# Kernel tuning notes

Hardware: AMD Instinct MI355X
Metric: run time of the kernel (lower is better)

## Reference

```python
import jax, jax.numpy as jnp
import numpy as np
from jax.ops import segment_sum

N_NODE, N_EDGE, D_IN, D_HID, N_CLS = 50000, 800000, 64, 64, 40


def setup_inputs() -> dict:
    key = jax.random.key(0)
    k1, k2, k3, k4 = jax.random.split(key, 4)
    x = jax.random.normal(k1, (N_NODE, D_IN), dtype=jnp.float32)
    edge_index = jax.random.randint(k2, (2, N_EDGE), 0, N_NODE, dtype=jnp.int64)
    W1 = jax.random.normal(k3, (D_IN, D_HID), dtype=jnp.float32) * (1.0 / np.sqrt(D_IN))
    b1 = jnp.zeros((D_HID,), dtype=jnp.float32)
    W2 = jax.random.normal(k4, (D_HID, N_CLS), dtype=jnp.float32) * (1.0 / np.sqrt(D_HID))
    b2 = jnp.zeros((N_CLS,), dtype=jnp.float32)
    return {"x": x, "edge_index": edge_index, "W1": W1, "b1": b1, "W2": W2, "b2": b2}


def _att_weights(fea, row, col, n):
    # edge-parallel cosine similarity (sklearn cosine_similarity restricted to edges)
    nrm = jnp.sqrt(jnp.sum(fea * fea, axis=1, keepdims=True))
    fn = fea / jnp.maximum(nrm, 1e-12)
    sim = jnp.sum(fn[row] * fn[col], axis=1)                 # [E]
    sim = jnp.where(sim < 0.1, 0.0, sim)                      # threshold
    # L1 row-normalization (sim >= 0 after threshold)
    rs = segment_sum(sim, row, num_segments=n)                # [N]
    sim_n = jnp.where(sim > 0, sim / jnp.maximum(rs[row], 1e-12), 0.0)
    # degree-based self-loop weight lam = 1/(deg+1)
    deg = segment_sum((sim > 0).astype(fea.dtype), row, num_segments=n)
    lam = 1.0 / (deg + 1.0)
    # exp applied only to stored (nonzero) entries; zeroed edges stay 0
    w_edge = jnp.where(sim > 0, jnp.exp(sim_n), 0.0)          # [E]
    w_self = jnp.exp(lam)                                     # [N] self-loop weights
    return w_edge, w_self


def _gcn(h, W, b, row, col, w_edge, w_self, n):
    # symmetric-norm GCN over weighted edges + explicit self loops
    deg = segment_sum(w_edge, row, num_segments=n) + w_self
    dinv = 1.0 / jnp.sqrt(jnp.maximum(deg, 1e-12))
    h = h @ W                                                 # [N, F]
    coef = w_edge * dinv[row] * dinv[col]                     # [E]
    out = segment_sum(coef[:, None] * h[col], row, num_segments=n)
    out = out + (w_self * dinv * dinv)[:, None] * h + b
    return out


def reference(x, edge_index, W1, b1, W2, b2):
    n = x.shape[0]
    row, col = edge_index[0], edge_index[1]
    # layer 1: attention coefs from raw features
    w1e, w1s = _att_weights(x, row, col, n)
    h = jax.nn.relu(_gcn(x, W1, b1, row, col, w1e, w1s, n))
    # layer 2: attention coefs recomputed on hidden features (dropout = eval mode)
    w2e, w2s = _att_weights(h, row, col, n)
    out = _gcn(h, W2, b2, row, col, w2e, w2s, n)
    return jax.nn.log_softmax(out, axis=1)
```

## Files before the change

kernel.cpp:

```cpp
#include <hip/hip_runtime.h>
#include <math.h>


#define ATT_CAP 96
#define EPB     2048
#define RPB     32
#define NBUCK_MAX 1600
#define CAPB    1024

typedef _Float16 half4 __attribute__((ext_vector_type(4)));

__global__ void k_bscat_norm_gemm(const int* __restrict__ row, const int* __restrict__ col,
                                  int* __restrict__ gcur, int* __restrict__ ebuf,
                                  int E, int nbuck, int nblkA, int nblkB,
                                  const float* __restrict__ x, float* __restrict__ fn,
                                  const float* __restrict__ W1, float* __restrict__ hd1,
                                  int N)
{
    __shared__ float smem[64 * 64 + 4 * 64];
    int b = blockIdx.x;
    int tid = threadIdx.x;
    if (b >= nblkA + nblkB) {
        float* sW = smem;
        float* sX = smem + 64 * 64;
        int gb = b - nblkA - nblkB;
        const float4* W4 = (const float4*)W1;
        float4* s4 = (float4*)sW;
#pragma unroll
        for (int i = 0; i < 4; ++i) s4[tid + 256 * i] = W4[tid + 256 * i];
        int base = gb * 4;
        {
            int rr = base + (tid >> 6);
            sX[tid] = (rr < N) ? x[(unsigned)rr * 64u + (unsigned)(tid & 63)] : 0.0f;
        }
        __syncthreads();
        int rl = tid >> 6, j = tid & 63;
        int r = base + rl;
        if (r < N) {
            float acc = 0.0f;
#pragma unroll
            for (int k = 0; k < 64; ++k) acc = fmaf(sX[rl * 64 + k], sW[k * 64 + j], acc);
            hd1[(unsigned)r * 64u + (unsigned)j] = acc;
        }
        return;
    }
    if (b >= nblkA) {
        int gid  = (b - nblkA) * blockDim.x + tid;
        int wid  = gid >> 6;
        int lane = tid & 63;
        if (wid >= N) return;
        float v = x[(unsigned)wid * 64u + (unsigned)lane];
        float s = v * v;
#pragma unroll
        for (int off = 32; off > 0; off >>= 1) s += __shfl_xor(s, off);
        float inv = rsqrtf(fmaxf(s, 1e-24f));
        fn[(unsigned)wid * 64u + (unsigned)lane] = v * inv;
        return;
    }
    int* lh    = (int*)smem;
    int* lbase = lh + NBUCK_MAX;
    int ebeg = b * EPB;
    int rr[8], cc[8];
    for (int i = tid; i < nbuck; i += blockDim.x) lh[i] = 0;
    __syncthreads();
#pragma unroll
    for (int k = 0; k < 8; ++k) {
        int e = ebeg + k * 256 + tid;
        bool v = (e < E);
        int r = v ? row[e] : -1;
        int c = v ? col[e] : 0;
        rr[k] = r; cc[k] = c;
        if (v) atomicAdd(&lh[r >> 5], 1);
    }
    __syncthreads();
    for (int i = tid; i < nbuck; i += blockDim.x) {
        int cnt = lh[i];
        if (cnt) lbase[i] = i * CAPB + atomicAdd(gcur + i, cnt);
        lh[i] = 0;
    }
    __syncthreads();
#pragma unroll
    for (int k = 0; k < 8; ++k) {
        int r = rr[k];
        if (r >= 0) {
            int j = r >> 5;
            int pos = lbase[j] + atomicAdd(&lh[j], 1);
            ebuf[pos] = ((r & (RPB - 1)) << 16) | cc[k];
        }
    }
}

__global__ void k_csr(const int* __restrict__ ebuf, const int* __restrict__ gcur,
                      int* __restrict__ rptr, int* __restrict__ col_s,
                      int N, int E, int nbuck)
{
    __shared__ int pk[CAPB];
    __shared__ int lcol[CAPB];
    __shared__ int lcnt[RPB], lexc[RPB], lcur[RPB];
    __shared__ int spart[4];
    int j = blockIdx.x;
    int tid = threadIdx.x;
    int lane = tid & 63, wave = tid >> 6;

    int part = 0;
    for (int i = tid; i < j; i += blockDim.x) part += gcur[i];
#pragma unroll
    for (int off = 32; off > 0; off >>= 1) part += __shfl_xor(part, off);
    if (lane == 0) spart[wave] = part;
    if (tid < RPB) lcnt[tid] = 0;
    __syncthreads();
    int beg = spart[0] + spart[1] + spart[2] + spart[3];
    int m = gcur[j]; if (m > CAPB) m = CAPB;

    const int* seg = ebuf + (size_t)j * CAPB;
    for (int i = tid; i < m; i += blockDim.x) pk[i] = seg[i];
    __syncthreads();
    for (int i = tid; i < m; i += blockDim.x) atomicAdd(&lcnt[pk[i] >> 16], 1);
    __syncthreads();
    if (tid < 32) {
        int a = lcnt[tid];
        int incl = a;
#pragma unroll
        for (int off = 1; off < 32; off <<= 1) {
            int v = __shfl_up(incl, off);
            if (tid >= off) incl += v;
        }
        lexc[tid] = incl - a;
        lcur[tid] = incl - a;
    }
    __syncthreads();
    for (int i = tid; i < m; i += blockDim.x) {
        int v = pk[i];
        int p = atomicAdd(&lcur[v >> 16], 1);
        lcol[p] = v & 0xFFFF;
    }
    __syncthreads();
    for (int i = tid; i < m; i += blockDim.x) col_s[beg + i] = lcol[i];
    if (tid < RPB) {
        int r = j * RPB + tid;
        if (r < N) rptr[r] = beg + lexc[tid];
    }
    if (j == 0 && tid == 0) rptr[N] = E;
}

__global__ void k_att(const float* __restrict__ fn,
                      const int* __restrict__ rptr, const int* __restrict__ col_s,
                      int2* __restrict__ cw, int* __restrict__ lend,
                      float* __restrict__ dinv, float* __restrict__ selfc,
                      const float* __restrict__ g2, _Float16* __restrict__ hd2,
                      float* __restrict__ hsc, int n)
{
    __shared__ float ssim[4][ATT_CAP];
    __shared__ int   scol[4][ATT_CAP];
    int wib  = threadIdx.x >> 6;
    int wid  = blockIdx.x * 4 + wib;
    int lane = threadIdx.x & 63;
    if (wid >= n) return;
    int sub = lane & 3;
    int grp = lane >> 2;
    int beg = rptr[wid], end = rptr[wid + 1];
    int deg_all = end - beg;

    const float4* frp = (const float4*)fn;
    unsigned rbase = (unsigned)wid * 16u;
    float4 a0 = frp[rbase + sub],     a1 = frp[rbase + sub + 4],
           a2 = frp[rbase + sub + 8], a3 = frp[rbase + sub + 12];

    float rs_part = 0.0f;
    int ngrp = (deg_all + 15) >> 4;
    for (int g = 0; g < ngrp; ++g) {
        int li = g * 16 + grp;
        float s = 0.0f; int c = 0;
        bool valid = (li < deg_all);
        if (valid) {
            c = col_s[beg + li];
            unsigned cb = (unsigned)c * 16u;
            float4 b0 = frp[cb + sub],     b1 = frp[cb + sub + 4],
                   b2 = frp[cb + sub + 8], b3 = frp[cb + sub + 12];
            float p = a0.x * b0.x + a0.y * b0.y + a0.z * b0.z + a0.w * b0.w
                    + a1.x * b1.x + a1.y * b1.y + a1.z * b1.z + a1.w * b1.w
                    + a2.x * b2.x + a2.y * b2.y + a2.z * b2.z + a2.w * b2.w
                    + a3.x * b3.x + a3.y * b3.y + a3.z * b3.z + a3.w * b3.w;
            p += __shfl_xor(p, 1);
            p += __shfl_xor(p, 2);
            s = (p < 0.1f) ? 0.0f : p;
        }
        if (sub == 0 && valid) {
            if (li < ATT_CAP) { ssim[wib][li] = s; scol[wib][li] = c; }
            if (s > 0.0f) rs_part += s;
        }
    }
#pragma unroll
    for (int off = 32; off > 0; off >>= 1) rs_part += __shfl_xor(rs_part, off);
    float denom = fmaxf(rs_part, 1e-12f);

    int   nlive = 0;
    float sw_lane = 0.0f;
    for (int base = 0; base < deg_all; base += 64) {
        int li = base + lane;
        bool valid = (li < deg_all);
        float s = 0.0f; int c = 0;
        if (valid) {
            if (li < ATT_CAP) { s = ssim[wib][li]; c = scol[wib][li]; }
            else {
                c = col_s[beg + li];
                const float* fr = fn + (size_t)wid * 64;
                const float* fc = fn + (size_t)c * 64;
                float p = 0.0f;
                for (int k = 0; k < 64; ++k) p += fr[k] * fc[k];
                s = (p < 0.1f) ? 0.0f : p;
            }
        }
        float w = (valid && s > 0.0f) ? __expf(s / denom) : 0.0f;
        unsigned long long M = __ballot(w > 0.0f);
        int rank = __popcll(M & ((1ull << lane) - 1ull));
        if (w > 0.0f) {
            int2 pw; pw.x = c; pw.y = __float_as_int(w);
            cw[beg + nlive + rank] = pw;
            sw_lane += w;
        }
        nlive += __popcll(M);
    }
#pragma unroll
    for (int off = 32; off > 0; off >>= 1) sw_lane += __shfl_xor(sw_lane, off);

    float wself = __expf(1.0f / ((float)nlive + 1.0f));
    float D  = sw_lane + wself;
    float di = rsqrtf(fmaxf(D, 1e-12f));
    if (lane == 0) {
        lend[wid]  = beg + nlive;
        dinv[wid]  = di;
        selfc[wid] = wself * di;
    }
    if (hsc)
        hsc[(unsigned)wid * 64u + (unsigned)lane] *= di;
    if (g2 && lane < 40)
        hd2[(unsigned)wid * 40u + (unsigned)lane] =
            (_Float16)(g2[(unsigned)wid * 40u + (unsigned)lane] * di);
}

template <int F, typename Vec4>
__device__ inline float agg_core_t(const Vec4* __restrict__ hdv,
                                   const int2* __restrict__ cw,
                                   int beg, int lend_, int lane)
{
    int q  = lane & 15;
    int eg = lane >> 4;
    bool qact = (F == 64) ? true : (q < (F >> 2));
    constexpr unsigned FQ = F >> 2;
    float acc0 = 0.f, acc1 = 0.f, acc2 = 0.f, acc3 = 0.f;
    for (int base = beg; base < lend_; base += 64) {
        int idx = base + lane;
        int cv = 0; float wv = 0.0f;
        if (idx < lend_) { int2 pw = cw[(unsigned)idx]; cv = pw.x; wv = __int_as_float(pw.y); }
        int cnt = lend_ - base; if (cnt > 64) cnt = 64;
        int nit = (cnt + 3) >> 2;

        Vec4  hv[4] = {};
        float wj[4] = {};
#pragma unroll
        for (int p = 0; p < 4; ++p) {
            int c = __shfl(cv, 4 * p + eg);
            wj[p] = __shfl(wv, 4 * p + eg);
            if (qact && p < nit) hv[p] = hdv[(unsigned)c * FQ + (unsigned)q];
        }
#pragma unroll
        for (int it = 0; it < 16; ++it) {
            if (it < nit) {
                float w = wj[it & 3];
                Vec4  h = hv[it & 3];
                acc0 += w * (float)h.x;
                acc1 += w * (float)h.y;
                acc2 += w * (float)h.z;
                acc3 += w * (float)h.w;
                if (it + 4 < nit) {
                    int jn = 4 * (it + 4);
                    int c = __shfl(cv, jn + eg);
                    wj[it & 3] = __shfl(wv, jn + eg);
                    if (qact) hv[it & 3] = hdv[(unsigned)c * FQ + (unsigned)q];
                }
            }
        }
    }
    acc0 += __shfl_xor(acc0, 16); acc0 += __shfl_xor(acc0, 32);
    acc1 += __shfl_xor(acc1, 16); acc1 += __shfl_xor(acc1, 32);
    acc2 += __shfl_xor(acc2, 16); acc2 += __shfl_xor(acc2, 32);
    acc3 += __shfl_xor(acc3, 16); acc3 += __shfl_xor(acc3, 32);
    int srcq = lane >> 2;
    float a0 = __shfl(acc0, srcq);
    float a1 = __shfl(acc1, srcq);
    float a2 = __shfl(acc2, srcq);
    float a3 = __shfl(acc3, srcq);
    int k = lane & 3;
    return (k == 0) ? a0 : (k == 1) ? a1 : (k == 2) ? a2 : a3;
}

__global__ void k_agg64(const float* __restrict__ hd, const int2* __restrict__ cw,
                        const float* __restrict__ dinv, const float* __restrict__ selfc,
                        const float* __restrict__ b, const int* __restrict__ row_ptr,
                        const int* __restrict__ lend, const float* __restrict__ W2,
                        float* __restrict__ g2, float* __restrict__ fnh, int n)
{
    __shared__ float sW2[64 * 40];
    __shared__ float sv[4][64];
    int tid = threadIdx.x;
    {
        const float4* W4 = (const float4*)W2;
        float4* s4 = (float4*)sW2;
        for (int i = tid; i < 64 * 40 / 4; i += 256) s4[i] = W4[i];
    }
    __syncthreads();

    int lane = tid & 63;
    int wib  = tid >> 6;
    float bl = b[lane];
    for (int t = 0; t < 2; ++t) {
        int wid = blockIdx.x * 8 + wib * 2 + t;
        if (wid >= n) break;
        int beg = row_ptr[wid], le = lend[wid];
        float hs = hd[(unsigned)wid * 64u + (unsigned)lane];
        float dv = dinv[wid];
        float sc = selfc[wid];
        float accf = agg_core_t<64>((const float4*)hd, cw, beg, le, lane);
        float v = dv * accf + sc * hs + bl;
        v = fmaxf(v, 0.0f);
        float s = v * v;
#pragma unroll
        for (int off = 32; off > 0; off >>= 1) s += __shfl_xor(s, off);
        float inv = rsqrtf(fmaxf(s, 1e-24f));
        fnh[(unsigned)wid * 64u + (unsigned)lane] = v * inv;

        sv[wib][lane] = v;
        if (lane < 40) {
            float acc = 0.0f;
#pragma unroll
            for (int k = 0; k < 64; ++k) acc = fmaf(sv[wib][k], sW2[k * 40 + lane], acc);
            g2[(unsigned)wid * 40u + (unsigned)lane] = acc;
        }
    }
}

__global__ void k_agg40_lsm(const _Float16* __restrict__ hd2, const int2* __restrict__ cw,
                            const float* __restrict__ dinv, const float* __restrict__ selfc,
                            const float* __restrict__ b, const int* __restrict__ row_ptr,
                            const int* __restrict__ lend,
                            float* __restrict__ out, int n)
{
    constexpr int F = 40;
    int gid  = blockIdx.x * blockDim.x + threadIdx.x;
    int wid  = gid >> 6;
    int lane = threadIdx.x & 63;
    if (wid >= n) return;
    int beg = row_ptr[wid], le = lend[wid];
    bool active = (lane < F);
    float hs = active ? (float)hd2[(unsigned)wid * 40u + (unsigned)lane] : 0.0f;
    float dv = dinv[wid];
    float sc = selfc[wid];
    float bl = active ? b[lane] : 0.0f;
    float accf = agg_core_t<F>((const half4*)hd2, cw, beg, le, lane);
    float v = 0.0f;
    if (active) v = dv * accf + sc * hs + bl;
    float m = active ? v : -__builtin_inff();
#pragma unroll
    for (int off = 32; off > 0; off >>= 1) m = fmaxf(m, __shfl_xor(m, off));
    float ex = active ? __expf(v - m) : 0.0f;
    float s = ex;
#pragma unroll
    for (int off = 32; off > 0; off >>= 1) s += __shfl_xor(s, off);
    if (active) out[(size_t)wid * F + lane] = v - m - __logf(s);
}

extern "C" void kernel_launch(void* const* d_in, const int* in_sizes, int n_in,
                              void* d_out, int out_size, void* d_ws, size_t ws_size,
                              hipStream_t stream)
{
    const float* x  = (const float*)d_in[0];
    const int*   ei = (const int*)d_in[1];
    const float* W1 = (const float*)d_in[2];
    const float* b1 = (const float*)d_in[3];
    const float* W2 = (const float*)d_in[4];
    const float* b2 = (const float*)d_in[5];
    float* out = (float*)d_out;

    const int N = in_sizes[0] / 64;
    const int E = in_sizes[1] / 2;
    const int* row = ei;
    const int* col = ei + E;

    const int nblkA = (E + EPB - 1) / EPB;
    const int nbuck = (N + RPB - 1) / RPB;

    char* p = (char*)d_ws;
    auto alloc = [&](size_t bytes) -> char* {
        char* r = p; p += (bytes + 255) & ~(size_t)255; return r;
    };
    float*     fn     = (float*)alloc((size_t)N * 64 * 4);
    float*     dinv   = (float*)alloc((size_t)N * 4);
    float*     selfc  = (float*)alloc((size_t)N * 4);
    float*     hd1    = (float*)alloc((size_t)N * 64 * 4);
    float*     g2     = (float*)alloc((size_t)N * 40 * 4);
    _Float16*  hd2    = (_Float16*)alloc((size_t)N * 40 * 2);
    float*     fnh    = (float*)alloc((size_t)N * 64 * 4);
    int*       rptr   = (int*)alloc((size_t)(N + 1) * 4);
    int*       lendv  = (int*)alloc((size_t)N * 4);
    int*       col_s  = (int*)alloc((size_t)E * 4);
    int2*      cw     = (int2*)alloc((size_t)E * 8);
    int*       ebuf   = (int*)alloc((size_t)nbuck * CAPB * 4);
    int*       gcur   = (int*)alloc((size_t)nbuck * 4);

    const int TB = 256;
    int blk_nodeWave = (N * 64 + TB - 1) / TB;
    int blk_gemm     = (N + 3) / 4;
    int blk_node4    = (N + 3) / 4;
    int blk_node8    = (N + 7) / 8;

    hipMemsetAsync(gcur, 0, (size_t)nbuck * 4, stream);

    k_bscat_norm_gemm<<<nblkA + blk_nodeWave + blk_gemm, TB, 0, stream>>>(
        row, col, gcur, ebuf, E, nbuck, nblkA, blk_nodeWave, x, fn, W1, hd1, N);
    k_csr<<<nbuck, TB, 0, stream>>>(ebuf, gcur, rptr, col_s, N, E, nbuck);

    k_att<<<blk_node4, TB, 0, stream>>>(fn, rptr, col_s, cw, lendv, dinv, selfc,
                                        (const float*)nullptr, (_Float16*)nullptr,
                                        hd1, N);
    k_agg64<<<blk_node8, TB, 0, stream>>>(hd1, cw, dinv, selfc, b1,
                                          rptr, lendv, W2, g2, fnh, N);

    k_att<<<blk_node4, TB, 0, stream>>>(fnh, rptr, col_s, cw, lendv, dinv, selfc,
                                        g2, hd2, (float*)nullptr, N);
    k_agg40_lsm<<<blk_nodeWave, TB, 0, stream>>>(hd2, cw, dinv, selfc, b2,
                                                 rptr, lendv, out, N);
}
```

Baseline: 255.7 us.

## Use fp16 feature copies for edge similarity and layer-1 aggregation gathers

```diff
diff --git a/kernel.cpp b/kernel.cpp
--- a/kernel.cpp
+++ b/kernel.cpp
@@ -9,15 +9,17 @@
 #define CAPB    1024
 
 typedef _Float16 half4 __attribute__((ext_vector_type(4)));
+typedef _Float16 half8 __attribute__((ext_vector_type(8)));
 
 __global__ void k_bscat_norm_gemm(const int* __restrict__ row, const int* __restrict__ col,
                                   int* __restrict__ gcur, int* __restrict__ ebuf,
                                   int E, int nbuck, int nblkA, int nblkB,
-                                  const float* __restrict__ x, float* __restrict__ fn,
+                                  const float* __restrict__ x,
+                                  _Float16* __restrict__ fn16, float* __restrict__ fn32,
                                   const float* __restrict__ W1, float* __restrict__ hd1,
                                   int N)
 {
-    __shared__ float smem[64 * 64 + 4 * 64];
+    __shared__ float smem[64 * 64 + 16 * 64];
     int b = blockIdx.x;
     int tid = threadIdx.x;
     if (b >= nblkA + nblkB) {
@@ -28,20 +30,31 @@
         float4* s4 = (float4*)sW;
 #pragma unroll
         for (int i = 0; i < 4; ++i) s4[tid + 256 * i] = W4[tid + 256 * i];
-        int base = gb * 4;
+        int base = gb * 16;
         {
-            int rr = base + (tid >> 6);
-            sX[tid] = (rr < N) ? x[(unsigned)rr * 64u + (unsigned)(tid & 63)] : 0.0f;
+            int rr = base + (tid >> 4);
+            int qq = tid & 15;
+            float4 v = {0.f, 0.f, 0.f, 0.f};
+            if (rr < N) v = ((const float4*)x)[(unsigned)rr * 16u + qq];
+            ((float4*)sX)[tid] = v;
         }
         __syncthreads();
-        int rl = tid >> 6, j = tid & 63;
-        int r = base + rl;
-        if (r < N) {
-            float acc = 0.0f;
-#pragma unroll
-            for (int k = 0; k < 64; ++k) acc = fmaf(sX[rl * 64 + k], sW[k * 64 + j], acc);
-            hd1[(unsigned)r * 64u + (unsigned)j] = acc;
-        }
+        int j = tid & 63;
+        int rl0 = (tid >> 6) * 4;
+        float a0 = 0.f, a1 = 0.f, a2 = 0.f, a3 = 0.f;
+#pragma unroll
+        for (int k = 0; k < 64; ++k) {
+            float w = sW[k * 64 + j];
+            a0 = fmaf(sX[(rl0 + 0) * 64 + k], w, a0);
+            a1 = fmaf(sX[(rl0 + 1) * 64 + k], w, a1);
+            a2 = fmaf(sX[(rl0 + 2) * 64 + k], w, a2);
+            a3 = fmaf(sX[(rl0 + 3) * 64 + k], w, a3);
+        }
+        int r0 = base + rl0;
+        if (r0 + 0 < N) hd1[(unsigned)(r0 + 0) * 64u + j] = a0;
+        if (r0 + 1 < N) hd1[(unsigned)(r0 + 1) * 64u + j] = a1;
+        if (r0 + 2 < N) hd1[(unsigned)(r0 + 2) * 64u + j] = a2;
+        if (r0 + 3 < N) hd1[(unsigned)(r0 + 3) * 64u + j] = a3;
         return;
     }
     if (b >= nblkA) {
@@ -54,7 +67,9 @@
 #pragma unroll
         for (int off = 32; off > 0; off >>= 1) s += __shfl_xor(s, off);
         float inv = rsqrtf(fmaxf(s, 1e-24f));
-        fn[(unsigned)wid * 64u + (unsigned)lane] = v * inv;
+        float vn = v * inv;
+        fn32[(unsigned)wid * 64u + (unsigned)lane] = vn;
+        fn16[(unsigned)wid * 64u + (unsigned)lane] = (_Float16)vn;
         return;
     }
     int* lh    = (int*)smem;
@@ -143,12 +158,13 @@
     if (j == 0 && tid == 0) rptr[N] = E;
 }
 
-__global__ void k_att(const float* __restrict__ fn,
+__global__ void k_att(const _Float16* __restrict__ fn16, const float* __restrict__ fn32,
                       const int* __restrict__ rptr, const int* __restrict__ col_s,
                       int2* __restrict__ cw, int* __restrict__ lend,
                       float* __restrict__ dinv, float* __restrict__ selfc,
                       const float* __restrict__ g2, _Float16* __restrict__ hd2,
-                      float* __restrict__ hsc, int n)
+                      const float* __restrict__ h1src, _Float16* __restrict__ h1dst,
+                      int n)
 {
     __shared__ float ssim[4][ATT_CAP];
     __shared__ int   scol[4][ATT_CAP];
@@ -161,10 +177,9 @@
     int beg = rptr[wid], end = rptr[wid + 1];
     int deg_all = end - beg;
 
-    const float4* frp = (const float4*)fn;
-    unsigned rbase = (unsigned)wid * 16u;
-    float4 a0 = frp[rbase + sub],     a1 = frp[rbase + sub + 4],
-           a2 = frp[rbase + sub + 8], a3 = frp[rbase + sub + 12];
+    const half8* frp = (const half8*)fn16;
+    unsigned rbase = (unsigned)wid * 8u;
+    half8 A0 = frp[rbase + sub], A1 = frp[rbase + sub + 4];
 
     float rs_part = 0.0f;
     int ngrp = (deg_all + 15) >> 4;
@@ -174,15 +189,26 @@
         bool valid = (li < deg_all);
         if (valid) {
             c = col_s[beg + li];
-            unsigned cb = (unsigned)c * 16u;
-            float4 b0 = frp[cb + sub],     b1 = frp[cb + sub + 4],
-                   b2 = frp[cb + sub + 8], b3 = frp[cb + sub + 12];
-            float p = a0.x * b0.x + a0.y * b0.y + a0.z * b0.z + a0.w * b0.w
-                    + a1.x * b1.x + a1.y * b1.y + a1.z * b1.z + a1.w * b1.w
-                    + a2.x * b2.x + a2.y * b2.y + a2.z * b2.z + a2.w * b2.w
-                    + a3.x * b3.x + a3.y * b3.y + a3.z * b3.z + a3.w * b3.w;
+            unsigned cb = (unsigned)c * 8u;
+            half8 B0 = frp[cb + sub], B1 = frp[cb + sub + 4];
+            float p = 0.0f;
+#pragma unroll
+            for (int i = 0; i < 8; ++i) p += (float)A0[i] * (float)B0[i];
+#pragma unroll
+            for (int i = 0; i < 8; ++i) p += (float)A1[i] * (float)B1[i];
             p += __shfl_xor(p, 1);
             p += __shfl_xor(p, 2);
+            if (fabsf(p - 0.1f) < 4e-3f) {
+                const float* fr = fn32 + (size_t)wid * 64;
+                const float* fc = fn32 + (size_t)c * 64;
+                float q = 0.0f;
+#pragma unroll
+                for (int k = 0; k < 16; ++k)
+                    q = fmaf(fr[sub * 16 + k], fc[sub * 16 + k], q);
+                q += __shfl_xor(q, 1);
+                q += __shfl_xor(q, 2);
+                p = q;
+            }
             s = (p < 0.1f) ? 0.0f : p;
         }
         if (sub == 0 && valid) {
@@ -204,8 +230,8 @@
             if (li < ATT_CAP) { s = ssim[wib][li]; c = scol[wib][li]; }
             else {
                 c = col_s[beg + li];
-                const float* fr = fn + (size_t)wid * 64;
-                const float* fc = fn + (size_t)c * 64;
+                const float* fr = fn32 + (size_t)wid * 64;
+                const float* fc = fn32 + (size_t)c * 64;
                 float p = 0.0f;
                 for (int k = 0; k < 64; ++k) p += fr[k] * fc[k];
                 s = (p < 0.1f) ? 0.0f : p;
@@ -232,8 +258,9 @@
         dinv[wid]  = di;
         selfc[wid] = wself * di;
     }
-    if (hsc)
-        hsc[(unsigned)wid * 64u + (unsigned)lane] *= di;
+    if (h1src)
+        h1dst[(unsigned)wid * 64u + (unsigned)lane] =
+            (_Float16)(h1src[(unsigned)wid * 64u + (unsigned)lane] * di);
     if (g2 && lane < 40)
         hd2[(unsigned)wid * 40u + (unsigned)lane] =
             (_Float16)(g2[(unsigned)wid * 40u + (unsigned)lane] * di);
@@ -295,11 +322,12 @@
     return (k == 0) ? a0 : (k == 1) ? a1 : (k == 2) ? a2 : a3;
 }
 
-__global__ void k_agg64(const float* __restrict__ hd, const int2* __restrict__ cw,
+__global__ void k_agg64(const _Float16* __restrict__ hd, const int2* __restrict__ cw,
                         const float* __restrict__ dinv, const float* __restrict__ selfc,
                         const float* __restrict__ b, const int* __restrict__ row_ptr,
                         const int* __restrict__ lend, const float* __restrict__ W2,
-                        float* __restrict__ g2, float* __restrict__ fnh, int n)
+                        float* __restrict__ g2,
+                        _Float16* __restrict__ fnh16, float* __restrict__ fnh32, int n)
 {
     __shared__ float sW2[64 * 40];
     __shared__ float sv[4][64];
@@ -318,17 +346,19 @@
         int wid = blockIdx.x * 8 + wib * 2 + t;
         if (wid >= n) break;
         int beg = row_ptr[wid], le = lend[wid];
-        float hs = hd[(unsigned)wid * 64u + (unsigned)lane];
+        float hs = (float)hd[(unsigned)wid * 64u + (unsigned)lane];
         float dv = dinv[wid];
         float sc = selfc[wid];
-        float accf = agg_core_t<64>((const float4*)hd, cw, beg, le, lane);
+        float accf = agg_core_t<64>((const half4*)hd, cw, beg, le, lane);
         float v = dv * accf + sc * hs + bl;
         v = fmaxf(v, 0.0f);
         float s = v * v;
 #pragma unroll
         for (int off = 32; off > 0; off >>= 1) s += __shfl_xor(s, off);
         float inv = rsqrtf(fmaxf(s, 1e-24f));
-        fnh[(unsigned)wid * 64u + (unsigned)lane] = v * inv;
+        float vn = v * inv;
+        fnh32[(unsigned)wid * 64u + (unsigned)lane] = vn;
+        fnh16[(unsigned)wid * 64u + (unsigned)lane] = (_Float16)vn;
 
         sv[wib][lane] = v;
         if (lane < 40) {
@@ -394,13 +424,16 @@
     auto alloc = [&](size_t bytes) -> char* {
         char* r = p; p += (bytes + 255) & ~(size_t)255; return r;
     };
-    float*     fn     = (float*)alloc((size_t)N * 64 * 4);
+    _Float16*  fn16   = (_Float16*)alloc((size_t)N * 64 * 2);
+    float*     fn32   = (float*)alloc((size_t)N * 64 * 4);
     float*     dinv   = (float*)alloc((size_t)N * 4);
     float*     selfc  = (float*)alloc((size_t)N * 4);
     float*     hd1    = (float*)alloc((size_t)N * 64 * 4);
+    _Float16*  hd1h   = (_Float16*)alloc((size_t)N * 64 * 2);
     float*     g2     = (float*)alloc((size_t)N * 40 * 4);
     _Float16*  hd2    = (_Float16*)alloc((size_t)N * 40 * 2);
-    float*     fnh    = (float*)alloc((size_t)N * 64 * 4);
+    _Float16*  fnh16  = (_Float16*)alloc((size_t)N * 64 * 2);
+    float*     fnh32  = (float*)alloc((size_t)N * 64 * 4);
     int*       rptr   = (int*)alloc((size_t)(N + 1) * 4);
     int*       lendv  = (int*)alloc((size_t)N * 4);
     int*       col_s  = (int*)alloc((size_t)E * 4);
@@ -410,24 +443,24 @@
 
     const int TB = 256;
     int blk_nodeWave = (N * 64 + TB - 1) / TB;
-    int blk_gemm     = (N + 3) / 4;
+    int blk_gemm     = (N + 15) / 16;
     int blk_node4    = (N + 3) / 4;
     int blk_node8    = (N + 7) / 8;
 
     hipMemsetAsync(gcur, 0, (size_t)nbuck * 4, stream);
 
     k_bscat_norm_gemm<<<nblkA + blk_nodeWave + blk_gemm, TB, 0, stream>>>(
-        row, col, gcur, ebuf, E, nbuck, nblkA, blk_nodeWave, x, fn, W1, hd1, N);
+        row, col, gcur, ebuf, E, nbuck, nblkA, blk_nodeWave, x, fn16, fn32, W1, hd1, N);
     k_csr<<<nbuck, TB, 0, stream>>>(ebuf, gcur, rptr, col_s, N, E, nbuck);
 
-    k_att<<<blk_node4, TB, 0, stream>>>(fn, rptr, col_s, cw, lendv, dinv, selfc,
+    k_att<<<blk_node4, TB, 0, stream>>>(fn16, fn32, rptr, col_s, cw, lendv, dinv, selfc,
                                         (const float*)nullptr, (_Float16*)nullptr,
-                                        hd1, N);
-    k_agg64<<<blk_node8, TB, 0, stream>>>(hd1, cw, dinv, selfc, b1,
-                                          rptr, lendv, W2, g2, fnh, N);
-
-    k_att<<<blk_node4, TB, 0, stream>>>(fnh, rptr, col_s, cw, lendv, dinv, selfc,
-                                        g2, hd2, (float*)nullptr, N);
+                                        hd1, hd1h, N);
+    k_agg64<<<blk_node8, TB, 0, stream>>>(hd1h, cw, dinv, selfc, b1,
+                                          rptr, lendv, W2, g2, fnh16, fnh32, N);
+
+    k_att<<<blk_node4, TB, 0, stream>>>(fnh16, fnh32, rptr, col_s, cw, lendv, dinv, selfc,
+                                        g2, hd2, (const float*)nullptr, (_Float16*)nullptr, N);
     k_agg40_lsm<<<blk_nodeWave, TB, 0, stream>>>(hd2, cw, dinv, selfc, b2,
                                                  rptr, lendv, out, N);
 }
```

Measured after the change: 463.5 us. +81.3%, slower.
